# Kernel optimization log

Hardware: AMD Instinct MI355X
Metric: run time of the kernel (lower is better)

The kernel has to match this reference:

```python
import jax, jax.numpy as jnp
import numpy as np

B, T, I, H = 64, 512, 256, 512


def setup_inputs() -> dict:
    key = jax.random.key(0)
    ks = jax.random.split(key, 3)
    x = jax.random.normal(ks[0], (B, T, I), dtype=jnp.float32)
    W = 0.1 * jax.random.normal(ks[1], (I, H), dtype=jnp.float32)
    U = 0.1 * jax.random.normal(ks[2], (H, H), dtype=jnp.float32)
    bias = jnp.ones((1, H), dtype=jnp.float32)
    alpha = jnp.full((1, 1), -3.0, dtype=jnp.float32)
    beta = jnp.full((1, 1), 3.0, dtype=jnp.float32)
    return {"x": x, "W": W, "U": U, "bias": bias, "alpha": alpha, "beta": beta}


def reference(x, W, U, bias, alpha, beta):
    # FastRNN: h_t = sigmoid(beta)*h_{t-1} + sigmoid(alpha)*tanh(W x_t + U h_{t-1} + b)
    sa = jax.nn.sigmoid(alpha)  # [1,1]
    sb = jax.nn.sigmoid(beta)   # [1,1]
    # Precompute input projection for all timesteps: [B,T,H]
    wx = jnp.einsum('bti,ih->bth', x, W)
    h0 = jnp.zeros((x.shape[0], U.shape[0]), dtype=x.dtype)

    def step(h, wx_t):
        pre = wx_t + h @ U + bias
        c = jnp.tanh(pre)
        h_new = sb * h + sa * c
        return h_new, h_new

    # scan over time: move T to leading axis
    _, hs = jax.lax.scan(step, h0, jnp.swapaxes(wx, 0, 1))
    return jnp.swapaxes(hs, 0, 1)  # [B,T,H]
```

## Files before the change

kernel.cpp:

```cpp
#include <hip/hip_runtime.h>
#include <stdint.h>


#define B_ 64
#define T_ 512
#define I_ 256
#define H_ 512
#define M_ (B_ * T_)
#define NSCAN 16

#define WXB_BYTES  ((size_t)M_ * H_ * 4)
#define HHALF_BYTES ((size_t)B_ * H_ * 2)

typedef short v8s __attribute__((ext_vector_type(8)));
typedef float v4f __attribute__((ext_vector_type(4)));
typedef unsigned long long u64t;

__device__ __forceinline__ uint16_t f2bf(float x) {
    union { float f; uint32_t u; } v; v.f = x;
    return (uint16_t)((v.u + 0x7FFFu + ((v.u >> 16) & 1u)) >> 16);
}

__global__ __launch_bounds__(256, 1) void rnn_fused(
        const float* __restrict__ x, const float* __restrict__ W,
        const float* __restrict__ U, const float* __restrict__ bias,
        const float* __restrict__ alpha, const float* __restrict__ beta,
        float* __restrict__ out, float* __restrict__ wxb,
        uint16_t* __restrict__ Hbuf) {
    __shared__ __align__(16) uint16_t smem[41984];

    const int tid = threadIdx.x;
    const int lane = tid & 63;
    const int w = tid >> 6;
    const int q = lane >> 4, c = lane & 15;

    if (blockIdx.x >= NSCAN) {
        const int gbid = (int)blockIdx.x - NSCAN;
        const int t0 = gbid >> 9, b = (gbid >> 3) & 63, n = gbid & 7;
        const int mbase = b * T_ + t0 * 64;
        const int nbase = n * 64;
        uint16_t (*Asl)[40] = (uint16_t(*)[40])smem;
        uint16_t* Bsl = smem + 64 * 40;

        v4f acc[4];
        #pragma unroll
        for (int i = 0; i < 4; ++i) acc[i] = (v4f){0.f, 0.f, 0.f, 0.f};

        for (int ks = 0; ks < I_; ks += 32) {
            {
                int row = tid >> 2, c4 = tid & 3;
                const float* gp = x + (size_t)(mbase + row) * I_ + ks + c4 * 8;
                float4 f0 = *(const float4*)gp;
                float4 f1 = *(const float4*)(gp + 4);
                uint16_t* dp = &Asl[row][c4 * 8];
                dp[0] = f2bf(f0.x); dp[1] = f2bf(f0.y); dp[2] = f2bf(f0.z); dp[3] = f2bf(f0.w);
                dp[4] = f2bf(f1.x); dp[5] = f2bf(f1.y); dp[6] = f2bf(f1.z); dp[7] = f2bf(f1.w);
            }
            {
                int nt = tid >> 6;
                const float* gp = W + (size_t)(ks + q * 8) * H_ + nbase + nt * 16 + c;
                union { v8s v; uint16_t u[8]; } pk;
                #pragma unroll
                for (int jj = 0; jj < 8; ++jj) pk.u[jj] = f2bf(gp[(size_t)jj * H_]);
                *(v8s*)&Bsl[(nt * 64 + lane) * 8] = pk.v;
            }
            __syncthreads();
            const v8s* Bf = (const v8s*)Bsl;
            v8s a = *(const v8s*)&Asl[w * 16 + c][q * 8];
            #pragma unroll
            for (int nt = 0; nt < 4; ++nt) {
                v8s bfr = Bf[nt * 64 + lane];
                acc[nt] = __builtin_amdgcn_mfma_f32_16x16x32_bf16(a, bfr, acc[nt], 0, 0, 0);
            }
            __syncthreads();
        }
        #pragma unroll
        for (int nt = 0; nt < 4; ++nt) {
            int j = nbase + nt * 16 + c;
            float bj = bias[j];
            #pragma unroll
            for (int r = 0; r < 4; ++r) {
                int m = mbase + w * 16 + q * 4 + r;
                union { float f; uint32_t u; } v; v.f = acc[nt][r] + bj;
                v.u |= 1u;
                __hip_atomic_store((uint32_t*)&wxb[(size_t)m * H_ + j], v.u,
                                   __ATOMIC_RELAXED, __HIP_MEMORY_SCOPE_AGENT);
            }
        }
        return;
    }

    auto& Als = *(uint16_t(*)[2][16][520])smem;

    const int bid = blockIdx.x;
    const int g = bid >> 2, s = bid & 3;

    float sa, sb;
    { float a = alpha[0], b = beta[0];
      sa = 1.f / (1.f + __expf(-a)); sb = 1.f / (1.f + __expf(-b)); }

    v8s Uf[2][16];
    #pragma unroll
    for (int nt = 0; nt < 2; ++nt) {
        int jg = s * 128 + (2 * w + nt) * 16 + c;
        #pragma unroll
        for (int slot = 0; slot < 16; ++slot) {
            int ktile = (slot < 12) ? (slot + ((slot >= (s << 2)) ? 4 : 0))
                                    : ((s << 2) + slot - 12);
            const float* gp = U + (size_t)(ktile * 32 + q * 8) * H_ + jg;
            union { v8s v; uint16_t u[8]; } pk;
            #pragma unroll
            for (int jj = 0; jj < 8; ++jj) pk.u[jj] = f2bf(gp[(size_t)jj * H_]);
            Uf[nt][slot] = pk.v;
        }
    }
    float hold[2][4];
    #pragma unroll
    for (int nt = 0; nt < 2; ++nt)
        #pragma unroll
        for (int r = 0; r < 4; ++r) hold[nt][r] = 0.f;

    float wxv[2][4], wxn[2][4];
    #pragma unroll
    for (int nt = 0; nt < 2; ++nt) {
        int jg = s * 128 + (2 * w + nt) * 16 + c;
        #pragma unroll
        for (int r = 0; r < 4; ++r) {
            int bg = g * 16 + q * 4 + r;
            uint32_t u = __hip_atomic_load(
                (const uint32_t*)&wxb[((size_t)bg * T_ + 0) * H_ + jg],
                __ATOMIC_RELAXED, __HIP_MEMORY_SCOPE_AGENT);
            wxn[nt][r] = __uint_as_float(u);
        }
    }

    const int prow = tid >> 4;
    size_t poffv[3];
    int pcolv[3];
    #pragma unroll
    for (int i = 0; i < 3; ++i) {
        int sp = i + ((i >= s) ? 1 : 0);
        pcolv[i] = sp * 128 + (tid & 15) * 8;
        poffv[i] = ((size_t)(g * 16 + prow)) * H_ + pcolv[i];
    }
    const int orow = tid >> 4;
    const int ocol = s * 128 + (tid & 15) * 8;
    const size_t ooff = ((size_t)(g * 16 + orow)) * H_ + ocol;

    #pragma unroll
    for (int u = 0; u < 8; ++u)
        *((u64t*)&Als[0][tid >> 4][0] + (tid & 15) * 8 + u) = 0;

    u64t ev[3][2];
    v4f accO0 = (v4f){0.f, 0.f, 0.f, 0.f};
    v4f accO1 = (v4f){0.f, 0.f, 0.f, 0.f};

    for (int t = 0; t < T_; ++t) {
        const int p = t & 1;
        #pragma unroll
        for (int nt = 0; nt < 2; ++nt)
            #pragma unroll
            for (int r = 0; r < 4; ++r) wxv[nt][r] = wxn[nt][r];

        if (t > 0) {
            const uint16_t* hbp = Hbuf + (size_t)p * (B_ * H_);
            const u64t lsb = 0x0001000100010001ull;
            const u64t want = ((t >> 1) & 1) ? lsb : 0ull;
            for (int guard = 0; guard < (1 << 20); ++guard) {
                u64t xx = (ev[0][0] ^ want) | (ev[0][1] ^ want)
                        | (ev[1][0] ^ want) | (ev[1][1] ^ want)
                        | (ev[2][0] ^ want) | (ev[2][1] ^ want);
                if (!(xx & lsb)) break;
                #pragma unroll
                for (int i = 0; i < 3; ++i) {
                    const u64t* gp = (const u64t*)(hbp + poffv[i]);
                    ev[i][0] = __hip_atomic_load(&gp[0], __ATOMIC_RELAXED,
                                                 __HIP_MEMORY_SCOPE_AGENT);
                    ev[i][1] = __hip_atomic_load(&gp[1], __ATOMIC_RELAXED,
                                                 __HIP_MEMORY_SCOPE_AGENT);
                }
            }
            #pragma unroll
            for (int i = 0; i < 3; ++i) {
                u64t* dp = (u64t*)&Als[p][prow][pcolv[i]];
                dp[0] = ev[i][0]; dp[1] = ev[i][1];
            }
        }
        __syncthreads();
        v4f acc0 = accO0;
        v4f acc1 = accO1;
        #pragma unroll
        for (int i = 0; i < 12; ++i) {
            int ktp = i + ((i >= (s << 2)) ? 4 : 0);
            v8s a = *(const v8s*)((const uint16_t*)&Als[p][c][0] + ktp * 32 + q * 8);
            acc0 = __builtin_amdgcn_mfma_f32_16x16x32_bf16(a, Uf[0][i], acc0, 0, 0, 0);
            acc1 = __builtin_amdgcn_mfma_f32_16x16x32_bf16(a, Uf[1][i], acc1, 0, 0, 0);
        }
        {
            for (int guard = 0; guard < (1 << 20); ++guard) {
                uint32_t andv = 0xFFFFFFFFu;
                #pragma unroll
                for (int nt = 0; nt < 2; ++nt)
                    #pragma unroll
                    for (int r = 0; r < 4; ++r)
                        andv &= __float_as_uint(wxv[nt][r]);
                if (andv & 1u) break;
                #pragma unroll
                for (int nt = 0; nt < 2; ++nt) {
                    int jg = s * 128 + (2 * w + nt) * 16 + c;
                    #pragma unroll
                    for (int r = 0; r < 4; ++r) {
                        int bg = g * 16 + q * 4 + r;
                        uint32_t u = __hip_atomic_load(
                            (const uint32_t*)&wxb[((size_t)bg * T_ + t) * H_ + jg],
                            __ATOMIC_RELAXED, __HIP_MEMORY_SCOPE_AGENT);
                        wxv[nt][r] = __uint_as_float(u);
                    }
                }
            }
        }
        const uint16_t tauw = (uint16_t)(((t + 1) >> 1) & 1);
        #pragma unroll
        for (int nt = 0; nt < 2; ++nt) {
            v4f av = nt ? acc1 : acc0;
            int jl = s * 128 + (2 * w + nt) * 16 + c;
            #pragma unroll
            for (int r = 0; r < 4; ++r) {
                float pre = av[r] + wxv[nt][r];
                float ex = __expf(pre + pre);
                float ct = 1.f - 2.f * __builtin_amdgcn_rcpf(ex + 1.f);
                float hn = sb * hold[nt][r] + sa * ct;
                hold[nt][r] = hn;
                Als[1 - p][q * 4 + r][jl] = (uint16_t)((f2bf(hn) & 0xFFFEu) | tauw);
            }
        }
        __syncthreads();
        if (t + 1 < T_) {
            {
                const u64t* sp = (const u64t*)&Als[1 - p][orow][ocol];
                u64t o0 = sp[0], o1 = sp[1];
                u64t* pp = (u64t*)(Hbuf + (size_t)(1 - p) * (B_ * H_) + ooff);
                __hip_atomic_store(&pp[0], o0, __ATOMIC_RELAXED,
                                   __HIP_MEMORY_SCOPE_AGENT);
                __hip_atomic_store(&pp[1], o1, __ATOMIC_RELAXED,
                                   __HIP_MEMORY_SCOPE_AGENT);
            }
            accO0 = (v4f){0.f, 0.f, 0.f, 0.f};
            accO1 = (v4f){0.f, 0.f, 0.f, 0.f};
            #pragma unroll
            for (int i = 0; i < 4; ++i) {
                int kto = (s << 2) + i;
                v8s a = *(const v8s*)((const uint16_t*)&Als[1 - p][c][0] + kto * 32 + q * 8);
                accO0 = __builtin_amdgcn_mfma_f32_16x16x32_bf16(a, Uf[0][12 + i], accO0, 0, 0, 0);
                accO1 = __builtin_amdgcn_mfma_f32_16x16x32_bf16(a, Uf[1][12 + i], accO1, 0, 0, 0);
            }
            #pragma unroll
            for (int nt = 0; nt < 2; ++nt) {
                int jg = s * 128 + (2 * w + nt) * 16 + c;
                #pragma unroll
                for (int r = 0; r < 4; ++r) {
                    int bg = g * 16 + q * 4 + r;
                    uint32_t u = __hip_atomic_load(
                        (const uint32_t*)&wxb[((size_t)bg * T_ + (t + 1)) * H_ + jg],
                        __ATOMIC_RELAXED, __HIP_MEMORY_SCOPE_AGENT);
                    wxn[nt][r] = __uint_as_float(u);
                }
            }
            const uint16_t* hbn = Hbuf + (size_t)(1 - p) * (B_ * H_);
            #pragma unroll
            for (int i = 0; i < 3; ++i) {
                const u64t* gp = (const u64t*)(hbn + poffv[i]);
                ev[i][0] = __hip_atomic_load(&gp[0], __ATOMIC_RELAXED,
                                             __HIP_MEMORY_SCOPE_AGENT);
                ev[i][1] = __hip_atomic_load(&gp[1], __ATOMIC_RELAXED,
                                             __HIP_MEMORY_SCOPE_AGENT);
            }
        }
        #pragma unroll
        for (int nt = 0; nt < 2; ++nt) {
            int jg = s * 128 + (2 * w + nt) * 16 + c;
            #pragma unroll
            for (int r = 0; r < 4; ++r) {
                int bg = g * 16 + q * 4 + r;
                out[((size_t)bg * T_ + t) * H_ + jg] = hold[nt][r];
            }
        }
    }
}

extern "C" void kernel_launch(void* const* d_in, const int* in_sizes, int n_in,
                              void* d_out, int out_size, void* d_ws, size_t ws_size,
                              hipStream_t stream) {
    const float* x     = (const float*)d_in[0];
    const float* W     = (const float*)d_in[1];
    const float* U     = (const float*)d_in[2];
    const float* bias  = (const float*)d_in[3];
    const float* alpha = (const float*)d_in[4];
    const float* beta  = (const float*)d_in[5];
    float* out = (float*)d_out;

    char* ws = (char*)d_ws;
    float* wxb = (float*)ws;
    uint16_t* Hbuf = (uint16_t*)(ws + WXB_BYTES);

    hipMemsetAsync(wxb, 0x00, WXB_BYTES, stream);
    hipMemsetAsync(Hbuf, 0x00, HHALF_BYTES, stream);
    hipMemsetAsync((char*)Hbuf + HHALF_BYTES, 0xFF, HHALF_BYTES, stream);

    rnn_fused<<<dim3(NSCAN + (M_ / 64) * (H_ / 64)), dim3(256), 0, stream>>>(
        x, W, U, bias, alpha, beta, out, wxb, Hbuf);
}
```

Before: 1.240 ms.

## Replace per-element wx flag polling with per-time-chunk completion counters

Input-projection blocks now write plain floats and, after a block barrier, bump a per-64-timestep counter with release semantics. Scan blocks wait once per chunk on that counter (acquire) and then use non-temporal loads for wx values. This drops the per-element tag bit, the per-step polling loop, and the large memset that cleared the wx buffer. In exchange, scan blocks stall at chunk boundaries until all 512 tiles of that chunk are finished, rather than waiting only for the specific elements they need.

```diff
diff --git a/kernel.cpp b/kernel.cpp
--- a/kernel.cpp
+++ b/kernel.cpp
@@ -21,12 +21,22 @@
     return (uint16_t)((v.u + 0x7FFFu + ((v.u >> 16) & 1u)) >> 16);
 }
 
+__device__ __forceinline__ void gate_chunk(const uint32_t* cnt, int k) {
+    for (int gd = 0; gd < (1 << 22); ++gd) {
+        uint32_t v = __hip_atomic_load(&cnt[k], __ATOMIC_RELAXED,
+                                       __HIP_MEMORY_SCOPE_AGENT);
+        if (v >= 512u) break;
+    }
+    (void)__hip_atomic_load(&cnt[k], __ATOMIC_ACQUIRE,
+                            __HIP_MEMORY_SCOPE_AGENT);
+}
+
 __global__ __launch_bounds__(256, 1) void rnn_fused(
         const float* __restrict__ x, const float* __restrict__ W,
         const float* __restrict__ U, const float* __restrict__ bias,
         const float* __restrict__ alpha, const float* __restrict__ beta,
         float* __restrict__ out, float* __restrict__ wxb,
-        uint16_t* __restrict__ Hbuf) {
+        uint16_t* __restrict__ Hbuf, uint32_t* __restrict__ cnt) {
     __shared__ __align__(16) uint16_t smem[41984];
 
     const int tid = threadIdx.x;
@@ -81,12 +91,13 @@
             #pragma unroll
             for (int r = 0; r < 4; ++r) {
                 int m = mbase + w * 16 + q * 4 + r;
-                union { float f; uint32_t u; } v; v.f = acc[nt][r] + bj;
-                v.u |= 1u;
-                __hip_atomic_store((uint32_t*)&wxb[(size_t)m * H_ + j], v.u,
-                                   __ATOMIC_RELAXED, __HIP_MEMORY_SCOPE_AGENT);
-            }
-        }
+                wxb[(size_t)m * H_ + j] = acc[nt][r] + bj;
+            }
+        }
+        __syncthreads();
+        if (tid == 0)
+            __hip_atomic_fetch_add(&cnt[t0], 1u, __ATOMIC_RELEASE,
+                                   __HIP_MEMORY_SCOPE_AGENT);
         return;
     }
 
@@ -120,6 +131,7 @@
         #pragma unroll
         for (int r = 0; r < 4; ++r) hold[nt][r] = 0.f;
 
+    gate_chunk(cnt, 0);
     float wxv[2][4], wxn[2][4];
     #pragma unroll
     for (int nt = 0; nt < 2; ++nt) {
@@ -127,10 +139,8 @@
         #pragma unroll
         for (int r = 0; r < 4; ++r) {
             int bg = g * 16 + q * 4 + r;
-            uint32_t u = __hip_atomic_load(
-                (const uint32_t*)&wxb[((size_t)bg * T_ + 0) * H_ + jg],
-                __ATOMIC_RELAXED, __HIP_MEMORY_SCOPE_AGENT);
-            wxn[nt][r] = __uint_as_float(u);
+            wxn[nt][r] = __builtin_nontemporal_load(
+                &wxb[((size_t)bg * T_ + 0) * H_ + jg]);
         }
     }
 
@@ -196,29 +206,6 @@
             acc0 = __builtin_amdgcn_mfma_f32_16x16x32_bf16(a, Uf[0][i], acc0, 0, 0, 0);
             acc1 = __builtin_amdgcn_mfma_f32_16x16x32_bf16(a, Uf[1][i], acc1, 0, 0, 0);
         }
-        {
-            for (int guard = 0; guard < (1 << 20); ++guard) {
-                uint32_t andv = 0xFFFFFFFFu;
-                #pragma unroll
-                for (int nt = 0; nt < 2; ++nt)
-                    #pragma unroll
-                    for (int r = 0; r < 4; ++r)
-                        andv &= __float_as_uint(wxv[nt][r]);
-                if (andv & 1u) break;
-                #pragma unroll
-                for (int nt = 0; nt < 2; ++nt) {
-                    int jg = s * 128 + (2 * w + nt) * 16 + c;
-                    #pragma unroll
-                    for (int r = 0; r < 4; ++r) {
-                        int bg = g * 16 + q * 4 + r;
-                        uint32_t u = __hip_atomic_load(
-                            (const uint32_t*)&wxb[((size_t)bg * T_ + t) * H_ + jg],
-                            __ATOMIC_RELAXED, __HIP_MEMORY_SCOPE_AGENT);
-                        wxv[nt][r] = __uint_as_float(u);
-                    }
-                }
-            }
-        }
         const uint16_t tauw = (uint16_t)(((t + 1) >> 1) & 1);
         #pragma unroll
         for (int nt = 0; nt < 2; ++nt) {
@@ -254,16 +241,15 @@
                 accO0 = __builtin_amdgcn_mfma_f32_16x16x32_bf16(a, Uf[0][12 + i], accO0, 0, 0, 0);
                 accO1 = __builtin_amdgcn_mfma_f32_16x16x32_bf16(a, Uf[1][12 + i], accO1, 0, 0, 0);
             }
+            if (((t + 1) & 63) == 0) gate_chunk(cnt, (t + 1) >> 6);
             #pragma unroll
             for (int nt = 0; nt < 2; ++nt) {
                 int jg = s * 128 + (2 * w + nt) * 16 + c;
                 #pragma unroll
                 for (int r = 0; r < 4; ++r) {
                     int bg = g * 16 + q * 4 + r;
-                    uint32_t u = __hip_atomic_load(
-                        (const uint32_t*)&wxb[((size_t)bg * T_ + (t + 1)) * H_ + jg],
-                        __ATOMIC_RELAXED, __HIP_MEMORY_SCOPE_AGENT);
-                    wxn[nt][r] = __uint_as_float(u);
+                    wxn[nt][r] = __builtin_nontemporal_load(
+                        &wxb[((size_t)bg * T_ + (t + 1)) * H_ + jg]);
                 }
             }
             const uint16_t* hbn = Hbuf + (size_t)(1 - p) * (B_ * H_);
@@ -302,11 +288,12 @@
     char* ws = (char*)d_ws;
     float* wxb = (float*)ws;
     uint16_t* Hbuf = (uint16_t*)(ws + WXB_BYTES);
-
-    hipMemsetAsync(wxb, 0x00, WXB_BYTES, stream);
+    uint32_t* cnt = (uint32_t*)(ws + WXB_BYTES + 2 * HHALF_BYTES);
+
     hipMemsetAsync(Hbuf, 0x00, HHALF_BYTES, stream);
     hipMemsetAsync((char*)Hbuf + HHALF_BYTES, 0xFF, HHALF_BYTES, stream);
+    hipMemsetAsync(cnt, 0x00, 8 * sizeof(uint32_t), stream);
 
     rnn_fused<<<dim3(NSCAN + (M_ / 64) * (H_ / 64)), dim3(256), 0, stream>>>(
-        x, W, U, bias, alpha, beta, out, wxb, Hbuf);
-}
+        x, W, U, bias, alpha, beta, out, wxb, Hbuf, cnt);
+}
```

Measured after the change: 1.221 ms. About the same (-1.5%).
